# Optimization experiments

Hardware: AMD Instinct MI355X
Metric: run time of the kernel (lower is better)

The kernel has to match this reference:

```python
import jax, jax.numpy as jnp
import numpy as np

B, T, N, F, H, R, E = 32, 8, 150, 16, 32, 4, 16


def _gconv(X, Af, Wf):
    # t-product graph conv (Kilmer t-product = circular conv over relation axis,
    # implemented facewise in the Fourier domain): ifft( fft(adj) @ fft(X) @ fft(W) )
    Xf = jnp.fft.fft(X, axis=-1)                      # [b,n,f,r] complex
    Y = jnp.einsum('nmr,bmfr->bnfr', Af, Xf)          # aggregate over nodes
    Y = jnp.einsum('bnfr,for->bnor', Y, Wf)           # feature transform
    return jnp.fft.ifft(Y, axis=-1).real


def _cell(X, Hs, Af, Wf, Bb):
    # TensorGRUCell. NOTE: faithful to the source, H_tilda reuses conv_hr
    # (conv_hh is defined but never used in the original forward).
    Wxz, Wxr, Wxh, Whz, Whr = Wf
    bz, br, bh = Bb[0], Bb[1], Bb[2]                  # [H,R], broadcasts over [b,n,H,R]
    Z = jax.nn.sigmoid(_gconv(X, Af, Wxz) + _gconv(Hs, Af, Whz) + bz)
    Rg = jax.nn.sigmoid(_gconv(X, Af, Wxr) + _gconv(Hs, Af, Whr) + br)
    Ht = jnp.tanh(_gconv(X, Af, Wxh) + _gconv(Rg * Hs, Af, Whr) + bh)
    return Z * Hs + (1.0 - Z) * Ht


def setup_inputs() -> dict:
    key = jax.random.key(0)
    ks = jax.random.split(key, 16)
    kai = lambda k, shp, fan: (jax.random.normal(k, shp, jnp.float32)
                               * np.float32(np.sqrt(2.0 / fan)))
    d = {}
    d['inputs'] = jax.random.normal(ks[0], (B, T, N, F, R), jnp.float32)
    d['U'] = kai(ks[1], (N, E, R), N)
    # layer 0 (input_dim=F)
    d['Wxz0'] = kai(ks[2], (F, H, R), F)
    d['Wxr0'] = kai(ks[3], (F, H, R), F)
    d['Wxh0'] = kai(ks[4], (F, H, R), F)
    d['Whz0'] = kai(ks[5], (H, H, R), H)
    d['Whr0'] = kai(ks[6], (H, H, R), H)
    d['B0'] = kai(ks[7], (3, H, R), 3)
    # layer 1 (input_dim=H)
    d['Wxz1'] = kai(ks[8], (H, H, R), H)
    d['Wxr1'] = kai(ks[9], (H, H, R), H)
    d['Wxh1'] = kai(ks[10], (H, H, R), H)
    d['Whz1'] = kai(ks[11], (H, H, R), H)
    d['Whr1'] = kai(ks[12], (H, H, R), H)
    d['B1'] = kai(ks[13], (3, H, R), 3)
    return d


def reference(inputs, U, Wxz0, Wxr0, Wxh0, Whz0, Whr0, B0,
              Wxz1, Wxr1, Wxh1, Whz1, Whr1, B1):
    # adaptive adjacency: softmax(relu(tprod(U, U^T)), dim=1)
    Uf = jnp.fft.fft(U, axis=-1)                      # [N,E,R] complex
    A = jnp.fft.ifft(jnp.einsum('ner,mer->nmr', Uf, Uf), axis=-1).real
    adj = jax.nn.softmax(jax.nn.relu(A), axis=1)      # [N,N,R]

    Af = jnp.fft.fft(adj, axis=-1)
    Wf0 = tuple(jnp.fft.fft(w, axis=-1) for w in (Wxz0, Wxr0, Wxh0, Whz0, Whr0))
    Wf1 = tuple(jnp.fft.fft(w, axis=-1) for w in (Wxz1, Wxr1, Wxh1, Whz1, Whr1))

    b, t, n, f, r = inputs.shape
    h = Whz0.shape[0]
    z0 = jnp.zeros((b, n, h, r), inputs.dtype)

    # t = 0: layer1 consumes the *current* layer0 output
    o0 = _cell(inputs[:, 0], z0, Af, Wf0, B0)
    o1 = _cell(o0, z0, Af, Wf1, B1)

    # t > 0: faithful to source, layer1 consumes the *previous timestep's*
    # layer0 output (temp_out[t-1][i-1]) with hidden temp_out[t-1][i].
    def step(carry, Xt):
        p0, p1 = carry
        n0 = _cell(Xt, p0, Af, Wf0, B0)
        n1 = _cell(p0, p1, Af, Wf1, B1)
        return (n0, n1), n1

    Xs = jnp.moveaxis(inputs[:, 1:], 1, 0)            # [T-1,B,N,F,R]
    (c0, c1), ys = jax.lax.scan(step, (o0, o1), Xs)

    out = jnp.concatenate([o1[None], ys], axis=0)     # [T,B,N,H,R]
    out = jnp.moveaxis(out, 0, 1)                     # [B,T,N,H,R]
    h_last = jnp.stack([c0, c1])                      # [L,B,N,H,R]
    return out, h_last
```

## Files before the change

kernel.cpp:

```cpp
#include <hip/hip_runtime.h>
#include <math.h>

#define NN 150
#define BB 32
#define TT 8
#define FF 16
#define HH 32
#define ROWS (NN*BB)
#define NCIN (BB*FF)
#define NCH  (BB*HH)
#define ADJ_LD 160
#define PS_LD 65

#define SZ_ADJF (4*NN*ADJ_LD)
#define SZ_WA0  (4*48*32*4)
#define SZ_WA1  (4*64*32*4)
#define SZ_WB   (32*32*4)
#define SZ_STATE (ROWS*HH*4)
#define SZ_PIN  (4*NN*NCIN)

__device__ __forceinline__ float sigmoidf_(float x){ return 1.f/(1.f+expf(-x)); }

__device__ __forceinline__ float comp_of4(float x0, float x1, float x2, float x3, int c) {
  return c==0 ? (x0+x1+x2+x3) : c==1 ? (x0-x2) : c==2 ? (x3-x1) : (x0-x1+x2-x3);
}


__global__ __launch_bounds__(256) void k_pre(
    const float* __restrict__ U, float* __restrict__ adjF,
    const float* __restrict__ Wxz0, const float* __restrict__ Wxr0, const float* __restrict__ Wxh0,
    const float* __restrict__ Whz0, const float* __restrict__ Whr0,
    const float* __restrict__ Wxz1, const float* __restrict__ Wxr1, const float* __restrict__ Wxh1,
    const float* __restrict__ Whz1, const float* __restrict__ Whr1,
    float* __restrict__ WA0p, float* __restrict__ WA1p,
    float* __restrict__ WB0p, float* __restrict__ WB1p) {
  __shared__ float Ufl[NN*16*4];
  __shared__ float Arow[NN*4];
  __shared__ float red[256];
  __shared__ float mxs[4], isms[4];
  int tid = threadIdx.x;
  if (blockIdx.x < NN) {
    int n = blockIdx.x;
    for (int idx = tid; idx < NN*16; idx += 256) {
      const float* s = U + (size_t)idx*4;
      float x0=s[0], x1=s[1], x2=s[2], x3=s[3];
      Ufl[idx*4+0] = x0+x1+x2+x3;
      Ufl[idx*4+1] = x0-x2;
      Ufl[idx*4+2] = x3-x1;
      Ufl[idx*4+3] = x0-x1+x2-x3;
    }
    __syncthreads();
    if (tid < NN) {
      int m = tid;
      float a0=0, ar=0, ai=0, a2=0;
      #pragma unroll
      for (int e = 0; e < 16; ++e) {
        const float* un = &Ufl[(n*16+e)*4];
        const float* um = &Ufl[(m*16+e)*4];
        a0 += un[0]*um[0];
        ar += un[1]*um[1] - un[2]*um[2];
        ai += un[1]*um[2] + un[2]*um[1];
        a2 += un[3]*um[3];
      }
      float r0 = 0.25f*(a0 + 2.f*ar + a2);
      float r1 = 0.25f*(a0 - 2.f*ai - a2);
      float r2 = 0.25f*(a0 - 2.f*ar + a2);
      float r3 = 0.25f*(a0 + 2.f*ai - a2);
      Arow[m*4+0] = fmaxf(r0, 0.f);
      Arow[m*4+1] = fmaxf(r1, 0.f);
      Arow[m*4+2] = fmaxf(r2, 0.f);
      Arow[m*4+3] = fmaxf(r3, 0.f);
    }
    __syncthreads();
    for (int r = 0; r < 4; ++r) {
      float v = (tid < NN) ? Arow[tid*4+r] : -1e30f;
      red[tid] = v; __syncthreads();
      for (int s = 128; s > 0; s >>= 1) { if (tid < s) red[tid] = fmaxf(red[tid], red[tid+s]); __syncthreads(); }
      if (tid == 0) mxs[r] = red[0];
      __syncthreads();
      float e = (tid < NN) ? expf(Arow[tid*4+r] - mxs[r]) : 0.f;
      red[tid] = e; __syncthreads();
      for (int s = 128; s > 0; s >>= 1) { if (tid < s) red[tid] += red[tid+s]; __syncthreads(); }
      if (tid == 0) isms[r] = 1.f / red[0];
      __syncthreads();
      if (tid < NN) Arow[tid*4+r] = e * isms[r];
      __syncthreads();
    }
    if (tid < NN) {
      int m = tid;
      float e0=Arow[m*4+0], e1=Arow[m*4+1], e2=Arow[m*4+2], e3=Arow[m*4+3];
      size_t base = (size_t)n*ADJ_LD + m;
      size_t cs = (size_t)NN*ADJ_LD;
      adjF[base]      = e0+e1+e2+e3;
      adjF[base+cs]   = e0-e2;
      adjF[base+2*cs] = e3-e1;
      adjF[base+3*cs] = e0-e1+e2-e3;
    } else if (tid < ADJ_LD) {
      size_t base = (size_t)n*ADJ_LD + tid;
      size_t cs = (size_t)NN*ADJ_LD;
      adjF[base] = 0.f; adjF[base+cs] = 0.f; adjF[base+2*cs] = 0.f; adjF[base+3*cs] = 0.f;
    }
    return;
  }
  int idx = (blockIdx.x - NN)*256 + tid;
  const float* src = nullptr;
  float* dst; int didx; int c;
  if (idx < SZ_WA0) {
    c = idx / 6144;
    int rem = idx % 6144;
    int k = rem >> 7, og = (rem >> 2) & 31, q = rem & 3;
    if (q == 0) src = (k < FF) ? Wxz0 + ((size_t)k*HH + og)*4 : Whz0 + ((size_t)(k-FF)*HH + og)*4;
    else if (q == 1) src = (k < FF) ? Wxr0 + ((size_t)k*HH + og)*4 : Whr0 + ((size_t)(k-FF)*HH + og)*4;
    else if (q == 2 && k < FF) src = Wxh0 + ((size_t)k*HH + og)*4;
    dst = WA0p; didx = idx;
  } else if (idx < SZ_WA0 + SZ_WA1) {
    int id = idx - SZ_WA0;
    c = id >> 13;
    int rem = id & 8191;
    int k = rem >> 7, og = (rem >> 2) & 31, q = rem & 3;
    if (q == 0) src = (k < HH) ? Wxz1 + ((size_t)k*HH + og)*4 : Whz1 + ((size_t)(k-HH)*HH + og)*4;
    else if (q == 1) src = (k < HH) ? Wxr1 + ((size_t)k*HH + og)*4 : Whr1 + ((size_t)(k-HH)*HH + og)*4;
    else if (q == 2 && k < HH) src = Wxh1 + ((size_t)k*HH + og)*4;
    dst = WA1p; didx = id;
  } else if (idx < SZ_WA0 + SZ_WA1 + SZ_WB) {
    int id = idx - (SZ_WA0 + SZ_WA1);
    int k = id >> 7, o = (id >> 2) & 31;
    c = id & 3;
    src = Whr0 + ((size_t)k*HH + o)*4;
    dst = WB0p; didx = id;
  } else if (idx < SZ_WA0 + SZ_WA1 + 2*SZ_WB) {
    int id = idx - (SZ_WA0 + SZ_WA1 + SZ_WB);
    int k = id >> 7, o = (id >> 2) & 31;
    c = id & 3;
    src = Whr1 + ((size_t)k*HH + o)*4;
    dst = WB1p; didx = id;
  } else return;
  float v0=0,v1=0,v2=0,v3=0;
  if (src) { v0=src[0]; v1=src[1]; v2=src[2]; v3=src[3]; }
  dst[didx] = comp_of4(v0,v1,v2,v3,c);
}

template<bool RAW>
__device__ __forceinline__ void agg_body(const float* __restrict__ adjF,
                                         const float* __restrict__ X,
                                         const float* __restrict__ inp,
                                         float* __restrict__ P, int ncol,
                                         int tile, int part, int rawt,
                                         float* As, float* Xs, int tid) {
  int kbeg = part ? 96 : 0;
  int kend = part ? NN : 96;
  int n0 = (tile % 5) * 32;
  int col0 = (tile / 5) * 32;
  int ti = tid & 31, tj = tid >> 5;
  int j0 = tj * 4;
  float a0[4]={}, aR[4]={}, aI[4]={}, a2v[4]={};
  float4 pa[4], px[4];

  #define LOAD_A(K0)                                                         \
    _Pragma("unroll")                                                        \
    for (int u = 0; u < 4; ++u) {                                            \
      int e = tid + u*256;                                                   \
      int c = e >> 8, rem = e & 255, i = rem >> 3, kq = rem & 7;             \
      int nn_ = n0 + i;                                                      \
      pa[u] = make_float4(0,0,0,0);                                          \
      if (nn_ < NN) pa[u] = *(const float4*)(adjF + ((size_t)c*NN + nn_)*ADJ_LD + (K0) + kq*4); \
    }
  #define STORE_A()                                                          \
    _Pragma("unroll")                                                        \
    for (int u = 0; u < 4; ++u) {                                            \
      int e = tid + u*256;                                                   \
      int c = e >> 8, rem = e & 255, i = rem >> 3, kq = rem & 7;             \
      As[((kq*4+0)*33 + i)*4 + c] = pa[u].x;                                 \
      As[((kq*4+1)*33 + i)*4 + c] = pa[u].y;                                 \
      As[((kq*4+2)*33 + i)*4 + c] = pa[u].z;                                 \
      As[((kq*4+3)*33 + i)*4 + c] = pa[u].w;                                 \
    }
  #define LOAD_X(K0)                                                         \
    if (RAW) {                                                               \
      int q = tid & 7, kk = tid >> 3;                                        \
      int mm = (K0) + kk;                                                    \
      int col = col0 + q*4;                                                  \
      int b = col >> 4, f = col & 15;                                        \
      px[0]=px[1]=px[2]=px[3]=make_float4(0,0,0,0);                          \
      if (mm < NN) {                                                         \
        const float* s = inp + (((size_t)(b*TT + rawt)*NN + mm)*FF + f)*4;   \
        px[0] = *(const float4*)(s+0);                                       \
        px[1] = *(const float4*)(s+4);                                       \
        px[2] = *(const float4*)(s+8);                                       \
        px[3] = *(const float4*)(s+12);                                      \
      }                                                                      \
    } else {                                                                 \
      _Pragma("unroll")                                                      \
      for (int u = 0; u < 4; ++u) {                                          \
        int e = tid + u*256;                                                 \
        int c = e >> 8, rem = e & 255, kk = rem >> 3, q = rem & 7;           \
        int mm = (K0) + kk;                                                  \
        px[u] = make_float4(0,0,0,0);                                        \
        if (mm < NN) px[u] = *(const float4*)(X + ((size_t)c*NN + mm)*ncol + col0 + q*4); \
      }                                                                      \
    }
  #define STORE_X()                                                          \
    if (RAW) {                                                               \
      int q = tid & 7, kk = tid >> 3;                                        \
      float4 r0 = px[0], r1 = px[1], r2 = px[2], r3 = px[3];                 \
      float4 w;                                                              \
      w = make_float4(r0.x+r0.y+r0.z+r0.w, r1.x+r1.y+r1.z+r1.w, r2.x+r2.y+r2.z+r2.w, r3.x+r3.y+r3.z+r3.w); \
      *(float4*)&Xs[(0*32+kk)*36 + q*4] = w;                                 \
      w = make_float4(r0.x-r0.z, r1.x-r1.z, r2.x-r2.z, r3.x-r3.z);           \
      *(float4*)&Xs[(1*32+kk)*36 + q*4] = w;                                 \
      w = make_float4(r0.w-r0.y, r1.w-r1.y, r2.w-r2.y, r3.w-r3.y);           \
      *(float4*)&Xs[(2*32+kk)*36 + q*4] = w;                                 \
      w = make_float4(r0.x-r0.y+r0.z-r0.w, r1.x-r1.y+r1.z-r1.w, r2.x-r2.y+r2.z-r2.w, r3.x-r3.y+r3.z-r3.w); \
      *(float4*)&Xs[(3*32+kk)*36 + q*4] = w;                                 \
    } else {                                                                 \
      _Pragma("unroll")                                                      \
      for (int u = 0; u < 4; ++u) {                                          \
        int e = tid + u*256;                                                 \
        int c = e >> 8, rem = e & 255, kk = rem >> 3, q = rem & 7;           \
        *(float4*)&Xs[(c*32+kk)*36 + q*4] = px[u];                           \
      }                                                                      \
    }

  LOAD_A(kbeg)
  LOAD_X(kbeg)
  for (int k0 = kbeg; k0 < kend; k0 += 32) {
    STORE_A()
    STORE_X()
    __syncthreads();
    int k0n = k0 + 32;
    if (k0n < kend) {
      LOAD_A(k0n)
      LOAD_X(k0n)
    }
    #pragma unroll 4
    for (int k = 0; k < 32; ++k) {
      float4 a4 = *(float4*)&As[(k*33 + ti)*4];
      float4 x0 = *(float4*)&Xs[(0*32+k)*36 + j0];
      float4 x1 = *(float4*)&Xs[(1*32+k)*36 + j0];
      float4 x2 = *(float4*)&Xs[(2*32+k)*36 + j0];
      float4 x3 = *(float4*)&Xs[(3*32+k)*36 + j0];
      float X0v[4]={x0.x,x0.y,x0.z,x0.w}, X1v[4]={x1.x,x1.y,x1.z,x1.w};
      float X2v[4]={x2.x,x2.y,x2.z,x2.w}, X3v[4]={x3.x,x3.y,x3.z,x3.w};
      #pragma unroll
      for (int j = 0; j < 4; ++j) {
        a0[j]  += a4.x*X0v[j];
        aR[j]  += a4.y*X1v[j] - a4.z*X2v[j];
        aI[j]  += a4.y*X2v[j] + a4.z*X1v[j];
        a2v[j] += a4.w*X3v[j];
      }
    }
    __syncthreads();
  }
  #undef LOAD_A
  #undef STORE_A
  #undef LOAD_X
  #undef STORE_X
  int nn_ = n0 + ti;
  if (nn_ < NN) {
    size_t cs = (size_t)NN*ncol;
    size_t rb = (size_t)nn_*ncol + col0 + j0;
    *(float4*)&P[rb]      = make_float4(a0[0],a0[1],a0[2],a0[3]);
    *(float4*)&P[rb+cs]   = make_float4(aR[0],aR[1],aR[2],aR[3]);
    *(float4*)&P[rb+2*cs] = make_float4(aI[0],aI[1],aI[2],aI[3]);
    *(float4*)&P[rb+3*cs] = make_float4(a2v[0],a2v[1],a2v[2],a2v[3]);
  }
}

#define AGG_AS 4224
#define AGG_XS 4608

__global__ __launch_bounds__(256,4) void k_aggIN(const float* __restrict__ adjF,
                                                 const float* __restrict__ inp,
                                                 float* __restrict__ PIN) {
  __shared__ float As[AGG_AS];
  __shared__ float Xs[AGG_XS];
  int u = blockIdx.x;
  int t = u / 160, rem = u % 160, part = rem / 80, tile = rem % 80;
  float* P = PIN + (size_t)t*2*SZ_PIN + (size_t)part*SZ_PIN;
  agg_body<true>(adjF, nullptr, inp, P, NCIN, tile, part, t, As, Xs, threadIdx.x);
}

struct AggParams {
  const float* X0; const float* X1;
  float* P0; float* P1;
  int base1, njobs, nb;
};
__global__ __launch_bounds__(256,4) void k_agg(AggParams pr, const float* __restrict__ adjF) {
  __shared__ float As[AGG_AS];
  __shared__ float Xs[AGG_XS];
  int bid = blockIdx.x;
  int part = (bid >= pr.nb) ? 1 : 0;
  if (part) bid -= pr.nb;
  const float* X; float* P; int tile;
  if (pr.njobs >= 2 && bid >= pr.base1) { X = pr.X1; P = pr.P1; tile = bid - pr.base1; }
  else { X = pr.X0; P = pr.P0; tile = bid; }
  P += (size_t)part * SZ_STATE;
  agg_body<false>(adjF, X, nullptr, P, NCH, tile, part, -1, As, Xs, threadIdx.x);
}

struct FAJob {
  const float* Px;
  const float* Ph;
  const float* W;
  const float* bias;
  const float* hprev;
  float* Z; float* T1; float* Mf;
  int zh;
};
struct FAParams { FAJob j[2]; };

template<int KTOT, int KX>
__device__ __forceinline__ void fusedA_body(const FAJob& jb, float* Ps, float* Ws) {
  const int row0 = blockIdx.x * 16;
  const int tid = threadIdx.x;
  const int og = tid & 31;
  const int rg = tid >> 5;
  const int r0 = rg*2, r1 = rg*2 + 1;
  const size_t psx = (size_t)4*ROWS*KX;
  const size_t psh = (size_t)4*ROWS*HH;
  constexpr int K4 = KTOT/4;
  for (int e = tid; e < 16*4*K4; e += 256) {
    int k4 = e % K4; int c = (e / K4) & 3; int r = e / (K4*4);
    int k = k4*4;
    int row = row0 + r;
    float4 v;
    if (k < KX) {
      const float* a = &jb.Px[((size_t)c*ROWS + row)*KX + k];
      float4 va = *(const float4*)a;
      float4 vb = *(const float4*)(a + psx);
      v = make_float4(va.x+vb.x, va.y+vb.y, va.z+vb.z, va.w+vb.w);
    } else if (jb.zh) {
      v = make_float4(0,0,0,0);
    } else {
      const float* a = &jb.Ph[((size_t)c*ROWS + row)*HH + (k - KX)];
      float4 va = *(const float4*)a;
      float4 vb = *(const float4*)(a + psh);
      v = make_float4(va.x+vb.x, va.y+vb.y, va.z+vb.z, va.w+vb.w);
    }
    Ps[(r*PS_LD + k+0)*4 + c] = v.x;
    Ps[(r*PS_LD + k+1)*4 + c] = v.y;
    Ps[(r*PS_LD + k+2)*4 + c] = v.z;
    Ps[(r*PS_LD + k+3)*4 + c] = v.w;
  }
  float acc0[2][3]={{0,0,0},{0,0,0}}, accR[2][3]={{0,0,0},{0,0,0}};
  float accI[2][3]={{0,0,0},{0,0,0}}, acc2[2][3]={{0,0,0},{0,0,0}};
  constexpr int NCHK = KTOT/16;
  const float4* Wg = (const float4*)jb.W;
  for (int cc = 0; cc < NCHK; ++cc) {
    __syncthreads();
    #pragma unroll
    for (int u = 0; u < 8; ++u) {
      int f = tid + u*256;
      int c = f >> 9, rem = f & 511;
      float4 v = Wg[((size_t)c*KTOT + cc*16)*32 + rem];
      *(float4*)&Ws[((size_t)c*512 + rem)*4] = v;
    }
    __syncthreads();
    #pragma unroll 4
    for (int kk = 0; kk < 16; ++kk) {
      int k = cc*16 + kk;
      float4 pA = *(float4*)&Ps[(r0*PS_LD + k)*4];
      float4 pB = *(float4*)&Ps[(r1*PS_LD + k)*4];
      float4 w0 = *(float4*)&Ws[((0*16+kk)*32+og)*4];
      float4 w1 = *(float4*)&Ws[((1*16+kk)*32+og)*4];
      float4 w2 = *(float4*)&Ws[((2*16+kk)*32+og)*4];
      float4 w3 = *(float4*)&Ws[((3*16+kk)*32+og)*4];
      float W0v[3]={w0.x,w0.y,w0.z}, W1v[3]={w1.x,w1.y,w1.z};
      float W2v[3]={w2.x,w2.y,w2.z}, W3v[3]={w3.x,w3.y,w3.z};
      #pragma unroll
      for (int q = 0; q < 3; ++q) {
        acc0[0][q] += pA.x*W0v[q];
        acc0[1][q] += pB.x*W0v[q];
        accR[0][q] += pA.y*W1v[q] - pA.z*W2v[q];
        accR[1][q] += pB.y*W1v[q] - pB.z*W2v[q];
        accI[0][q] += pA.y*W2v[q] + pA.z*W1v[q];
        accI[1][q] += pB.y*W2v[q] + pB.z*W1v[q];
        acc2[0][q] += pA.w*W3v[q];
        acc2[1][q] += pB.w*W3v[q];
      }
    }
  }
  const float* bz = jb.bias + (0*HH + og)*4;
  const float* br = jb.bias + (1*HH + og)*4;
  const float* bh = jb.bias + (2*HH + og)*4;
  float bzv[4] = {bz[0],bz[1],bz[2],bz[3]};
  float brv[4] = {br[0],br[1],br[2],br[3]};
  float bhv[4] = {bh[0],bh[1],bh[2],bh[3]};
  #pragma unroll
  for (int rr = 0; rr < 2; ++rr) {
    int row = row0 + rg*2 + rr;
    float ys[3][4];
    #pragma unroll
    for (int q = 0; q < 3; ++q) {
      float Y0 = acc0[rr][q], Yr = accR[rr][q], Yi = accI[rr][q], Y2 = acc2[rr][q];
      ys[q][0] = 0.25f*(Y0 + 2.f*Yr + Y2);
      ys[q][1] = 0.25f*(Y0 - 2.f*Yi - Y2);
      ys[q][2] = 0.25f*(Y0 - 2.f*Yr + Y2);
      ys[q][3] = 0.25f*(Y0 + 2.f*Yi - Y2);
    }
    float4 z = make_float4(sigmoidf_(ys[0][0]+bzv[0]), sigmoidf_(ys[0][1]+bzv[1]),
                           sigmoidf_(ys[0][2]+bzv[2]), sigmoidf_(ys[0][3]+bzv[3]));
    *(float4*)&jb.Z[((size_t)row*HH + og)*4] = z;
    float4 hp = make_float4(0,0,0,0);
    if (!jb.zh) hp = *(const float4*)&jb.hprev[((size_t)row*HH + og)*4];
    float m0 = sigmoidf_(ys[1][0]+brv[0]) * hp.x;
    float m1 = sigmoidf_(ys[1][1]+brv[1]) * hp.y;
    float m2 = sigmoidf_(ys[1][2]+brv[2]) * hp.z;
    float m3 = sigmoidf_(ys[1][3]+brv[3]) * hp.w;
    size_t mb = (size_t)row*HH + og;
    size_t cs = (size_t)ROWS*HH;
    jb.Mf[mb]      = m0+m1+m2+m3;
    jb.Mf[mb+cs]   = m0-m2;
    jb.Mf[mb+2*cs] = m3-m1;
    jb.Mf[mb+3*cs] = m0-m1+m2-m3;
    float4 tv = make_float4(ys[2][0]+bhv[0], ys[2][1]+bhv[1], ys[2][2]+bhv[2], ys[2][3]+bhv[3]);
    *(float4*)&jb.T1[((size_t)row*HH + og)*4] = tv;
  }
}

#define FA_PS (16*PS_LD*4)

__global__ __launch_bounds__(256,3) void k_fusedA_both(FAParams pr) {
  __shared__ float Ps[FA_PS];
  __shared__ float Ws[8192];
  if (blockIdx.y == 0) fusedA_body<48,16>(pr.j[0], Ps, Ws);
  else                 fusedA_body<64,32>(pr.j[1], Ps, Ws);
}
__global__ __launch_bounds__(256,3) void k_fusedA_L0(FAParams pr) {
  __shared__ float Ps[FA_PS];
  __shared__ float Ws[8192];
  fusedA_body<48,16>(pr.j[0], Ps, Ws);
}
__global__ __launch_bounds__(256,3) void k_fusedA_L1(FAParams pr) {
  __shared__ float Ps[FA_PS];
  __shared__ float Ws[8192];
  fusedA_body<64,32>(pr.j[1], Ps, Ws);
}

struct FBJob {
  const float* Pm; const float* W; const float* T1; const float* Z;
  float* h; float* hf; float* outp; float* hlast;
  int t, zh, wout;
};
struct FBParams { FBJob j[2]; };
__global__ __launch_bounds__(256,4) void k_fusedB(FBParams pr) {
  __shared__ float Ps[16*32*4];
  __shared__ float Ws[32*32*4];
  FBJob jb = pr.j[blockIdx.y];
  int row0 = blockIdx.x * 16;
  int tid = threadIdx.x;
  int rg = tid >> 5, o = tid & 31;
  int r0 = rg*2, r1 = r0 + 1;
  float acc0[2]={0,0}, accR[2]={0,0}, accI[2]={0,0}, acc2[2]={0,0};
  if (!jb.zh) {
    #pragma unroll
    for (int u = 0; u < 4; ++u) {
      int f = tid + u*256;
      ((float4*)Ws)[f] = ((const float4*)jb.W)[f];
    }
    const size_t psh = (size_t)4*ROWS*HH;
    #pragma unroll
    for (int u = 0; u < 2; ++u) {
      int e = tid + u*256;
      int r = e >> 5, k = e & 31;
      int row = row0 + r;
      float4 v;
      float* vv = (float*)&v;
      #pragma unroll
      for (int c = 0; c < 4; ++c) {
        size_t ix = ((size_t)c*ROWS + row)*HH + k;
        vv[c] = jb.Pm[ix] + jb.Pm[ix + psh];
      }
      *(float4*)&Ps[(r*32 + k)*4] = v;
    }
    __syncthreads();
    #pragma unroll 8
    for (int k = 0; k < 32; ++k) {
      float4 pA = *(const float4*)&Ps[(r0*32 + k)*4];
      float4 pB = *(const float4*)&Ps[(r1*32 + k)*4];
      float4 w  = *(const float4*)&Ws[(k*32 + o)*4];
      acc0[0] += pA.x*w.x;  acc0[1] += pB.x*w.x;
      accR[0] += pA.y*w.y - pA.z*w.z;  accR[1] += pB.y*w.y - pB.z*w.z;
      accI[0] += pA.y*w.z + pA.z*w.y;  accI[1] += pB.y*w.z + pB.z*w.y;
      acc2[0] += pA.w*w.w;  acc2[1] += pB.w*w.w;
    }
  }
  #pragma unroll
  for (int rr = 0; rr < 2; ++rr) {
    int row = row0 + rg*2 + rr;
    float y0 = 0.25f*(acc0[rr] + 2.f*accR[rr] + acc2[rr]);
    float y1 = 0.25f*(acc0[rr] - 2.f*accI[rr] - acc2[rr]);
    float y2 = 0.25f*(acc0[rr] - 2.f*accR[rr] + acc2[rr]);
    float y3 = 0.25f*(acc0[rr] + 2.f*accI[rr] - acc2[rr]);
    float4 t1 = *(const float4*)&jb.T1[((size_t)row*HH + o)*4];
    float h0v = tanhf(t1.x + y0);
    float h1v = tanhf(t1.y + y1);
    float h2v = tanhf(t1.z + y2);
    float h3v = tanhf(t1.w + y3);
    float4 z = *(const float4*)&jb.Z[((size_t)row*HH + o)*4];
    float4 hp = make_float4(0,0,0,0);
    if (!jb.zh) hp = *(const float4*)&jb.h[((size_t)row*HH + o)*4];
    float n0v = z.x*hp.x + (1.f-z.x)*h0v;
    float n1v = z.y*hp.y + (1.f-z.y)*h1v;
    float n2v = z.z*hp.z + (1.f-z.z)*h2v;
    float n3v = z.w*hp.w + (1.f-z.w)*h3v;
    *(float4*)&jb.h[((size_t)row*HH + o)*4] = make_float4(n0v,n1v,n2v,n3v);
    size_t hb = (size_t)row*HH + o, cs = (size_t)ROWS*HH;
    jb.hf[hb]      = n0v+n1v+n2v+n3v;
    jb.hf[hb+cs]   = n0v-n2v;
    jb.hf[hb+2*cs] = n3v-n1v;
    jb.hf[hb+3*cs] = n0v-n1v+n2v-n3v;
    int n = row >> 5, b = row & 31;
    if (jb.wout) {
      float* dst = jb.outp + (((size_t)b*TT + jb.t)*NN + n)*(HH*4) + o*4;
      *(float4*)dst = make_float4(n0v,n1v,n2v,n3v);
    }
    if (jb.hlast) {
      float* dst = jb.hlast + ((size_t)(b*NN + n))*(HH*4) + o*4;
      *(float4*)dst = make_float4(n0v,n1v,n2v,n3v);
    }
  }
}

extern "C" void kernel_launch(void* const* d_in, const int* in_sizes, int n_in,
                              void* d_out, int out_size, void* d_ws, size_t ws_size,
                              hipStream_t stream) {
  const float* inp  = (const float*)d_in[0];
  const float* U    = (const float*)d_in[1];
  const float* Wxz0 = (const float*)d_in[2];
  const float* Wxr0 = (const float*)d_in[3];
  const float* Wxh0 = (const float*)d_in[4];
  const float* Whz0 = (const float*)d_in[5];
  const float* Whr0 = (const float*)d_in[6];
  const float* B0   = (const float*)d_in[7];
  const float* Wxz1 = (const float*)d_in[8];
  const float* Wxr1 = (const float*)d_in[9];
  const float* Wxh1 = (const float*)d_in[10];
  const float* Whz1 = (const float*)d_in[11];
  const float* Whr1 = (const float*)d_in[12];
  const float* B1   = (const float*)d_in[13];
  float* out = (float*)d_out;

  float* ws = (float*)d_ws;
  float* ADJF = ws;  ws += SZ_ADJF;
  float* WA0  = ws;  ws += SZ_WA0;
  float* WA1  = ws;  ws += SZ_WA1;
  float* WB0  = ws;  ws += SZ_WB;
  float* WB1  = ws;  ws += SZ_WB;
  float* H0   = ws;  ws += SZ_STATE;
  float* H1   = ws;  ws += SZ_STATE;
  float* H0F  = ws;  ws += SZ_STATE;
  float* H1F  = ws;  ws += SZ_STATE;
  float* PIN  = ws;  ws += (size_t)TT*2*SZ_PIN;
  float* PH0  = ws;  ws += 2*SZ_STATE;
  float* PH1  = ws;  ws += 2*SZ_STATE;
  float* PM0  = ws;  ws += 2*SZ_STATE;
  float* PM1  = ws;  ws += 2*SZ_STATE;
  float* M0F  = ws;  ws += SZ_STATE;
  float* M1F  = ws;  ws += SZ_STATE;
  float* Z0   = ws;  ws += SZ_STATE;
  float* Z1   = ws;  ws += SZ_STATE;
  float* T10  = ws;  ws += SZ_STATE;
  float* T11  = ws;  ws += SZ_STATE;

  k_pre<<<NN + (SZ_WA0+SZ_WA1+2*SZ_WB+255)/256, 256, 0, stream>>>(
      U, ADJF, Wxz0,Wxr0,Wxh0,Whz0,Whr0, Wxz1,Wxr1,Wxh1,Whz1,Whr1, WA0,WA1,WB0,WB1);

  k_aggIN<<<TT*2*80, 256, 0, stream>>>(ADJF, inp, PIN);

  float* hlast0 = out + (size_t)BB*TT*NN*HH*4;
  float* hlast1 = hlast0 + (size_t)BB*NN*HH*4;

  {
    FAParams p;
    p.j[0] = FAJob{PIN, nullptr, WA0, B0, nullptr, Z0, T10, M0F, 1};
    p.j[1] = p.j[0];
    k_fusedA_L0<<<dim3(300,1), 256, 0, stream>>>(p);
  }
  {
    FBParams p;
    p.j[0] = FBJob{nullptr, WB0, T10, Z0, H0, H0F, nullptr, nullptr, 0, 1, 0};
    p.j[1] = p.j[0];
    k_fusedB<<<dim3(300,1), 256, 0, stream>>>(p);
  }
  {
    AggParams p; p.X0=H0F; p.P0=PH0; p.X1=nullptr; p.P1=nullptr;
    p.base1=0; p.njobs=1; p.nb=160;
    k_agg<<<320, 256, 0, stream>>>(p, ADJF);
  }
  {
    FAParams p;
    p.j[0] = FAJob{PH0, nullptr, WA1, B1, nullptr, Z1, T11, M1F, 1};
    p.j[1] = p.j[0];
    k_fusedA_L1<<<dim3(300,1), 256, 0, stream>>>(p);
  }
  {
    FBParams p;
    p.j[0] = FBJob{nullptr, WB1, T11, Z1, H1, H1F, out, nullptr, 0, 1, 1};
    p.j[1] = p.j[0];
    k_fusedB<<<dim3(300,1), 256, 0, stream>>>(p);
  }

  for (int t = 1; t < TT; ++t) {
    {
      AggParams p; p.X0=H0F; p.P0=PH0; p.X1=H1F; p.P1=PH1;
      p.base1=160; p.njobs=2; p.nb=320;
      k_agg<<<640, 256, 0, stream>>>(p, ADJF);
    }
    {
      FAParams p;
      p.j[0] = FAJob{PIN + (size_t)t*2*SZ_PIN, PH0, WA0, B0, H0, Z0, T10, M0F, 0};
      p.j[1] = FAJob{PH0, PH1, WA1, B1, H1, Z1, T11, M1F, 0};
      k_fusedA_both<<<dim3(300,2), 256, 0, stream>>>(p);
    }
    {
      AggParams p; p.X0=M0F; p.P0=PM0; p.X1=M1F; p.P1=PM1;
      p.base1=160; p.njobs=2; p.nb=320;
      k_agg<<<640, 256, 0, stream>>>(p, ADJF);
    }
    {
      int last = (t == TT-1);
      FBParams p;
      p.j[0] = FBJob{PM0, WB0, T10, Z0, H0, H0F, nullptr, last ? hlast0 : nullptr, t, 0, 0};
      p.j[1] = FBJob{PM1, WB1, T11, Z1, H1, H1F, out,     last ? hlast1 : nullptr, t, 0, 1};
      k_fusedB<<<dim3(300,2), 256, 0, stream>>>(p);
    }
  }
}
```

Measured before the change: 830.2 us.

## Fuse per-timestep node aggregation with gate GEMMs into two kernels

Each recurrent timestep now runs two fused kernels instead of four. Each one computes the Fourier-domain adjacency aggregation for a 16-node by one-batch tile in shared memory and immediately applies the feature-transform GEMMs and gate nonlinearities for both layers. This removes the global round trips of the partial aggregation buffers and two launches per step. The cost is a full-K aggregation per block without the earlier split-K parallelism, only 320 blocks, lower occupancy (launch bounds of 2) and heavier shared-memory use.

Result: slower. 1.019 ms (+22.8%).

```diff
diff --git a/kernel.cpp b/kernel.cpp
--- a/kernel.cpp
+++ b/kernel.cpp
@@ -281,9 +281,7 @@
 }
 
 struct AggParams {
-  const float* X0; const float* X1;
-  float* P0; float* P1;
-  int base1, njobs, nb;
+  const float* X0; float* P0; int nb;
 };
 __global__ __launch_bounds__(256,4) void k_agg(AggParams pr, const float* __restrict__ adjF) {
   __shared__ float As[AGG_AS];
@@ -291,18 +289,12 @@
   int bid = blockIdx.x;
   int part = (bid >= pr.nb) ? 1 : 0;
   if (part) bid -= pr.nb;
-  const float* X; float* P; int tile;
-  if (pr.njobs >= 2 && bid >= pr.base1) { X = pr.X1; P = pr.P1; tile = bid - pr.base1; }
-  else { X = pr.X0; P = pr.P0; tile = bid; }
-  P += (size_t)part * SZ_STATE;
-  agg_body<false>(adjF, X, nullptr, P, NCH, tile, part, -1, As, Xs, threadIdx.x);
+  float* P = pr.P0 + (size_t)part * SZ_STATE;
+  agg_body<false>(adjF, pr.X0, nullptr, P, NCH, bid, part, -1, As, Xs, threadIdx.x);
 }
 
 struct FAJob {
-  const float* Px;
-  const float* Ph;
-  const float* W;
-  const float* bias;
+  const float* Px; const float* Ph; const float* W; const float* bias;
   const float* hprev;
   float* Z; float* T1; float* Mf;
   int zh;
@@ -420,12 +412,6 @@
 
 #define FA_PS (16*PS_LD*4)
 
-__global__ __launch_bounds__(256,3) void k_fusedA_both(FAParams pr) {
-  __shared__ float Ps[FA_PS];
-  __shared__ float Ws[8192];
-  if (blockIdx.y == 0) fusedA_body<48,16>(pr.j[0], Ps, Ws);
-  else                 fusedA_body<64,32>(pr.j[1], Ps, Ws);
-}
 __global__ __launch_bounds__(256,3) void k_fusedA_L0(FAParams pr) {
   __shared__ float Ps[FA_PS];
   __shared__ float Ws[8192];
@@ -522,6 +508,294 @@
   }
 }
 
+#define SMEM_STEP 11392
+
+__device__ __forceinline__ void step_agg(const float* __restrict__ adjF,
+    const float* __restrict__ X0g, const float* __restrict__ X1g,
+    int n0, int b, int tid, float* smem) {
+  float* As  = smem;
+  float* Xs0 = smem + 2176;
+  float* Xs1 = smem + 6784;
+  int an = tid & 15, hg = (tid >> 4) & 7, job = tid >> 7;
+  int h0 = hg * 4;
+  const float* Xsj = job ? Xs1 : Xs0;
+  float a0[4]={}, aR[4]={}, aI[4]={}, a2[4]={};
+  float4 pa[2], px[8];
+
+  #define SLOAD(K0)                                                          \
+    { _Pragma("unroll") for (int u = 0; u < 2; ++u) {                        \
+        int e = tid + u*256;                                                 \
+        int c = e >> 7, rem = e & 127, i = rem >> 3, kq = rem & 7;           \
+        int nn_ = n0 + i;                                                    \
+        pa[u] = make_float4(0,0,0,0);                                        \
+        if (nn_ < NN) pa[u] = *(const float4*)(adjF + ((size_t)c*NN + nn_)*ADJ_LD + (K0) + kq*4); \
+      }                                                                      \
+      _Pragma("unroll") for (int u = 0; u < 8; ++u) {                        \
+        int e = tid + u*256;                                                 \
+        int jj = e >> 10, rem = e & 1023, c = rem >> 8, rem2 = rem & 255;    \
+        int kk = rem2 >> 3, q = rem2 & 7;                                    \
+        int m = (K0) + kk;                                                   \
+        const float* Xg = jj ? X1g : X0g;                                    \
+        px[u] = make_float4(0,0,0,0);                                       \
+        if (m < NN) px[u] = *(const float4*)(Xg + ((size_t)c*NN + m)*NCH + b*32 + q*4); \
+      } }
+  #define SSTORE()                                                           \
+    { _Pragma("unroll") for (int u = 0; u < 2; ++u) {                        \
+        int e = tid + u*256;                                                 \
+        int c = e >> 7, rem = e & 127, i = rem >> 3, kq = rem & 7;           \
+        As[((kq*4+0)*17 + i)*4 + c] = pa[u].x;                               \
+        As[((kq*4+1)*17 + i)*4 + c] = pa[u].y;                               \
+        As[((kq*4+2)*17 + i)*4 + c] = pa[u].z;                               \
+        As[((kq*4+3)*17 + i)*4 + c] = pa[u].w;                               \
+      }                                                                      \
+      _Pragma("unroll") for (int u = 0; u < 8; ++u) {                        \
+        int e = tid + u*256;                                                 \
+        int jj = e >> 10, rem = e & 1023, c = rem >> 8, rem2 = rem & 255;    \
+        int kk = rem2 >> 3, q = rem2 & 7;                                    \
+        float* Xsd = jj ? Xs1 : Xs0;                                         \
+        *(float4*)&Xsd[(c*32+kk)*36 + q*4] = px[u];                          \
+      } }
+
+  SLOAD(0)
+  for (int k0 = 0; k0 < 160; k0 += 32) {
+    SSTORE()
+    __syncthreads();
+    if (k0 + 32 < 160) SLOAD(k0+32)
+    #pragma unroll 4
+    for (int k = 0; k < 32; ++k) {
+      float4 a4 = *(float4*)&As[(k*17 + an)*4];
+      float4 x0 = *(float4*)&Xsj[(0*32+k)*36 + h0];
+      float4 x1 = *(float4*)&Xsj[(1*32+k)*36 + h0];
+      float4 x2 = *(float4*)&Xsj[(2*32+k)*36 + h0];
+      float4 x3 = *(float4*)&Xsj[(3*32+k)*36 + h0];
+      float X0v[4]={x0.x,x0.y,x0.z,x0.w}, X1v[4]={x1.x,x1.y,x1.z,x1.w};
+      float X2v[4]={x2.x,x2.y,x2.z,x2.w}, X3v[4]={x3.x,x3.y,x3.z,x3.w};
+      #pragma unroll
+      for (int j = 0; j < 4; ++j) {
+        a0[j] += a4.x*X0v[j];
+        aR[j] += a4.y*X1v[j] - a4.z*X2v[j];
+        aI[j] += a4.y*X2v[j] + a4.z*X1v[j];
+        a2[j] += a4.w*X3v[j];
+      }
+    }
+    __syncthreads();
+  }
+  #undef SLOAD
+  #undef SSTORE
+  float* PsH = smem + job*2112;
+  #pragma unroll
+  for (int j = 0; j < 4; ++j)
+    *(float4*)&PsH[(an*33 + h0 + j)*4] = make_float4(a0[j], aR[j], aI[j], a2[j]);
+}
+
+template<int KTOT, int KXA>
+__device__ __forceinline__ void s1_pass(const float* __restrict__ Wraw,
+    const float* __restrict__ bias, const float* __restrict__ hprev,
+    float* __restrict__ Z, float* __restrict__ T1, float* __restrict__ Mf,
+    const float* PsA, int stA, const float* PsB, int stB,
+    float* Ws, int n0, int b, int tid) {
+  const float4* Wg = (const float4*)Wraw;
+  int og = tid & 31, rg = tid >> 5;
+  float acc0[2][3]={{0,0,0},{0,0,0}}, accR[2][3]={{0,0,0},{0,0,0}};
+  float accI[2][3]={{0,0,0},{0,0,0}}, acc2[2][3]={{0,0,0},{0,0,0}};
+  constexpr int NCHK = KTOT/8;
+  for (int cc = 0; cc < NCHK; ++cc) {
+    __syncthreads();
+    #pragma unroll
+    for (int u = 0; u < 4; ++u) {
+      int f = tid + u*256;
+      int c = f >> 8, rem = f & 255, kk = rem >> 5, o = rem & 31;
+      float4 v = Wg[((size_t)c*KTOT + cc*8 + kk)*32 + o];
+      *(float4*)&Ws[((c*8+kk)*32 + o)*4] = v;
+    }
+    __syncthreads();
+    const float* pb; int st, ko;
+    if (cc*8 < KXA) { pb = PsA; st = stA; ko = 0; }
+    else            { pb = PsB; st = stB; ko = KXA; }
+    #pragma unroll 2
+    for (int kk = 0; kk < 8; ++kk) {
+      int k = cc*8 + kk;
+      float4 w0 = *(float4*)&Ws[((0*8+kk)*32+og)*4];
+      float4 w1 = *(float4*)&Ws[((1*8+kk)*32+og)*4];
+      float4 w2 = *(float4*)&Ws[((2*8+kk)*32+og)*4];
+      float4 w3 = *(float4*)&Ws[((3*8+kk)*32+og)*4];
+      float W0v[3]={w0.x,w0.y,w0.z}, W1v[3]={w1.x,w1.y,w1.z};
+      float W2v[3]={w2.x,w2.y,w2.z}, W3v[3]={w3.x,w3.y,w3.z};
+      #pragma unroll
+      for (int rr = 0; rr < 2; ++rr) {
+        int r = rg*2 + rr;
+        float4 p = *(const float4*)&pb[r*st + (k-ko)*4];
+        #pragma unroll
+        for (int q = 0; q < 3; ++q) {
+          acc0[rr][q] += p.x*W0v[q];
+          accR[rr][q] += p.y*W1v[q] - p.z*W2v[q];
+          accI[rr][q] += p.y*W2v[q] + p.z*W1v[q];
+          acc2[rr][q] += p.w*W3v[q];
+        }
+      }
+    }
+  }
+  const float* bz = bias + (0*HH + og)*4;
+  const float* br = bias + (1*HH + og)*4;
+  const float* bh = bias + (2*HH + og)*4;
+  float bzv[4] = {bz[0],bz[1],bz[2],bz[3]};
+  float brv[4] = {br[0],br[1],br[2],br[3]};
+  float bhv[4] = {bh[0],bh[1],bh[2],bh[3]};
+  #pragma unroll
+  for (int rr = 0; rr < 2; ++rr) {
+    int n = n0 + rg*2 + rr;
+    if (n >= NN) continue;
+    int row = n*BB + b;
+    float ys[3][4];
+    #pragma unroll
+    for (int q = 0; q < 3; ++q) {
+      float Y0 = acc0[rr][q], Yr = accR[rr][q], Yi = accI[rr][q], Y2 = acc2[rr][q];
+      ys[q][0] = 0.25f*(Y0 + 2.f*Yr + Y2);
+      ys[q][1] = 0.25f*(Y0 - 2.f*Yi - Y2);
+      ys[q][2] = 0.25f*(Y0 - 2.f*Yr + Y2);
+      ys[q][3] = 0.25f*(Y0 + 2.f*Yi - Y2);
+    }
+    float4 z = make_float4(sigmoidf_(ys[0][0]+bzv[0]), sigmoidf_(ys[0][1]+bzv[1]),
+                           sigmoidf_(ys[0][2]+bzv[2]), sigmoidf_(ys[0][3]+bzv[3]));
+    *(float4*)&Z[((size_t)row*HH + og)*4] = z;
+    float4 hp = *(const float4*)&hprev[((size_t)row*HH + og)*4];
+    float m0 = sigmoidf_(ys[1][0]+brv[0]) * hp.x;
+    float m1 = sigmoidf_(ys[1][1]+brv[1]) * hp.y;
+    float m2 = sigmoidf_(ys[1][2]+brv[2]) * hp.z;
+    float m3 = sigmoidf_(ys[1][3]+brv[3]) * hp.w;
+    size_t mb = (size_t)row*HH + og;
+    size_t cs = (size_t)ROWS*HH;
+    Mf[mb]      = m0+m1+m2+m3;
+    Mf[mb+cs]   = m0-m2;
+    Mf[mb+2*cs] = m3-m1;
+    Mf[mb+3*cs] = m0-m1+m2-m3;
+    float4 tv = make_float4(ys[2][0]+bhv[0], ys[2][1]+bhv[1], ys[2][2]+bhv[2], ys[2][3]+bhv[3]);
+    *(float4*)&T1[((size_t)row*HH + og)*4] = tv;
+  }
+}
+
+struct S1Params {
+  const float* adjF; const float* PINt;
+  const float* H0F; const float* H1F;
+  const float* WA0; const float* WA1;
+  const float* B0; const float* B1;
+  const float* H0; const float* H1;
+  float* Z0; float* T10; float* M0F;
+  float* Z1; float* T11; float* M1F;
+};
+
+__global__ __launch_bounds__(256,2) void k_step1(S1Params p) {
+  __shared__ float smem[SMEM_STEP];
+  int tid = threadIdx.x;
+  int nt = blockIdx.x % 10, b = blockIdx.x / 10;
+  int n0 = nt * 16;
+  step_agg(p.adjF, p.H0F, p.H1F, n0, b, tid, smem);
+  {
+    int c = tid >> 6, rem = tid & 63, nl = rem >> 2, fq = rem & 3;
+    float4 v = make_float4(0,0,0,0);
+    if (n0 + nl < NN) {
+      const float* a = p.PINt + ((size_t)c*NN + n0+nl)*NCIN + b*16 + fq*4;
+      float4 va = *(const float4*)a;
+      float4 vb = *(const float4*)(a + SZ_PIN);
+      v = make_float4(va.x+vb.x, va.y+vb.y, va.z+vb.z, va.w+vb.w);
+    }
+    float* PsIN = smem + 4224;
+    PsIN[(nl*16 + fq*4+0)*4 + c] = v.x;
+    PsIN[(nl*16 + fq*4+1)*4 + c] = v.y;
+    PsIN[(nl*16 + fq*4+2)*4 + c] = v.z;
+    PsIN[(nl*16 + fq*4+3)*4 + c] = v.w;
+  }
+  float* Ws = smem + 5248;
+  s1_pass<48,16>(p.WA0, p.B0, p.H0, p.Z0, p.T10, p.M0F,
+                 smem + 4224, 64, smem, 132, Ws, n0, b, tid);
+  s1_pass<64,32>(p.WA1, p.B1, p.H1, p.Z1, p.T11, p.M1F,
+                 smem, 132, smem + 2112, 132, Ws, n0, b, tid);
+}
+
+__device__ __forceinline__ void s2_pass(const float* __restrict__ WBg,
+    const float* __restrict__ T1g, const float* __restrict__ Zg,
+    float* __restrict__ h, float* __restrict__ hf,
+    float* __restrict__ outp, float* __restrict__ hlast, int t,
+    const float* PsM, float* Ws, int n0, int b, int tid) {
+  int og = tid & 31, rg = tid >> 5;
+  __syncthreads();
+  #pragma unroll
+  for (int u = 0; u < 4; ++u) {
+    int f = tid + u*256;
+    ((float4*)Ws)[f] = ((const float4*)WBg)[f];
+  }
+  __syncthreads();
+  float acc0[2]={0,0}, accR[2]={0,0}, accI[2]={0,0}, acc2[2]={0,0};
+  #pragma unroll 4
+  for (int k = 0; k < 32; ++k) {
+    float4 w = *(const float4*)&Ws[(k*32 + og)*4];
+    #pragma unroll
+    for (int rr = 0; rr < 2; ++rr) {
+      int r = rg*2 + rr;
+      float4 pm = *(const float4*)&PsM[(r*33 + k)*4];
+      acc0[rr] += pm.x*w.x;
+      accR[rr] += pm.y*w.y - pm.z*w.z;
+      accI[rr] += pm.y*w.z + pm.z*w.y;
+      acc2[rr] += pm.w*w.w;
+    }
+  }
+  #pragma unroll
+  for (int rr = 0; rr < 2; ++rr) {
+    int n = n0 + rg*2 + rr;
+    if (n >= NN) continue;
+    int row = n*BB + b;
+    float y0 = 0.25f*(acc0[rr] + 2.f*accR[rr] + acc2[rr]);
+    float y1 = 0.25f*(acc0[rr] - 2.f*accI[rr] - acc2[rr]);
+    float y2 = 0.25f*(acc0[rr] - 2.f*accR[rr] + acc2[rr]);
+    float y3 = 0.25f*(acc0[rr] + 2.f*accI[rr] - acc2[rr]);
+    float4 t1 = *(const float4*)&T1g[((size_t)row*HH + og)*4];
+    float h0v = tanhf(t1.x + y0);
+    float h1v = tanhf(t1.y + y1);
+    float h2v = tanhf(t1.z + y2);
+    float h3v = tanhf(t1.w + y3);
+    float4 z = *(const float4*)&Zg[((size_t)row*HH + og)*4];
+    float4 hp = *(const float4*)&h[((size_t)row*HH + og)*4];
+    float n0v = z.x*hp.x + (1.f-z.x)*h0v;
+    float n1v = z.y*hp.y + (1.f-z.y)*h1v;
+    float n2v = z.z*hp.z + (1.f-z.z)*h2v;
+    float n3v = z.w*hp.w + (1.f-z.w)*h3v;
+    *(float4*)&h[((size_t)row*HH + og)*4] = make_float4(n0v,n1v,n2v,n3v);
+    size_t hb = (size_t)row*HH + og, cs = (size_t)ROWS*HH;
+    hf[hb]      = n0v+n1v+n2v+n3v;
+    hf[hb+cs]   = n0v-n2v;
+    hf[hb+2*cs] = n3v-n1v;
+    hf[hb+3*cs] = n0v-n1v+n2v-n3v;
+    if (outp) {
+      float* dst = outp + (((size_t)b*TT + t)*NN + n)*(HH*4) + og*4;
+      *(float4*)dst = make_float4(n0v,n1v,n2v,n3v);
+    }
+    if (hlast) {
+      float* dst = hlast + ((size_t)(b*NN + n))*(HH*4) + og*4;
+      *(float4*)dst = make_float4(n0v,n1v,n2v,n3v);
+    }
+  }
+}
+
+struct S2Params {
+  const float* adjF; const float* M0F; const float* M1F;
+  const float* WB0; const float* WB1;
+  const float* T10; const float* Z0; const float* T11; const float* Z1;
+  float* H0; float* H1; float* H0F; float* H1F;
+  float* outp; float* hlast0; float* hlast1;
+  int t;
+};
+
+__global__ __launch_bounds__(256,2) void k_step2(S2Params p) {
+  __shared__ float smem[SMEM_STEP];
+  int tid = threadIdx.x;
+  int nt = blockIdx.x % 10, b = blockIdx.x / 10;
+  int n0 = nt * 16;
+  step_agg(p.adjF, p.M0F, p.M1F, n0, b, tid, smem);
+  float* Ws = smem + 4224;
+  s2_pass(p.WB0, p.T10, p.Z0, p.H0, p.H0F, nullptr, p.hlast0, p.t, smem,        Ws, n0, b, tid);
+  s2_pass(p.WB1, p.T11, p.Z1, p.H1, p.H1F, p.outp,  p.hlast1, p.t, smem + 2112, Ws, n0, b, tid);
+}
+
 extern "C" void kernel_launch(void* const* d_in, const int* in_sizes, int n_in,
                               void* d_out, int out_size, void* d_ws, size_t ws_size,
                               hipStream_t stream) {
@@ -553,9 +827,6 @@
   float* H1F  = ws;  ws += SZ_STATE;
   float* PIN  = ws;  ws += (size_t)TT*2*SZ_PIN;
   float* PH0  = ws;  ws += 2*SZ_STATE;
-  float* PH1  = ws;  ws += 2*SZ_STATE;
-  float* PM0  = ws;  ws += 2*SZ_STATE;
-  float* PM1  = ws;  ws += 2*SZ_STATE;
   float* M0F  = ws;  ws += SZ_STATE;
   float* M1F  = ws;  ws += SZ_STATE;
   float* Z0   = ws;  ws += SZ_STATE;
@@ -584,14 +855,13 @@
     k_fusedB<<<dim3(300,1), 256, 0, stream>>>(p);
   }
   {
-    AggParams p; p.X0=H0F; p.P0=PH0; p.X1=nullptr; p.P1=nullptr;
-    p.base1=0; p.njobs=1; p.nb=160;
+    AggParams p; p.X0 = H0F; p.P0 = PH0; p.nb = 160;
     k_agg<<<320, 256, 0, stream>>>(p, ADJF);
   }
   {
     FAParams p;
-    p.j[0] = FAJob{PH0, nullptr, WA1, B1, nullptr, Z1, T11, M1F, 1};
-    p.j[1] = p.j[0];
+    p.j[0] = FAJob{PIN, nullptr, WA0, B0, nullptr, Z0, T10, M0F, 1};
+    p.j[1] = FAJob{PH0, nullptr, WA1, B1, nullptr, Z1, T11, M1F, 1};
     k_fusedA_L1<<<dim3(300,1), 256, 0, stream>>>(p);
   }
   {
@@ -603,27 +873,27 @@
 
   for (int t = 1; t < TT; ++t) {
     {
-      AggParams p; p.X0=H0F; p.P0=PH0; p.X1=H1F; p.P1=PH1;
-      p.base1=160; p.njobs=2; p.nb=320;
-      k_agg<<<640, 256, 0, stream>>>(p, ADJF);
-    }
-    {
-      FAParams p;
-      p.j[0] = FAJob{PIN + (size_t)t*2*SZ_PIN, PH0, WA0, B0, H0, Z0, T10, M0F, 0};
-      p.j[1] = FAJob{PH0, PH1, WA1, B1, H1, Z1, T11, M1F, 0};
-      k_fusedA_both<<<dim3(300,2), 256, 0, stream>>>(p);
-    }
-    {
-      AggParams p; p.X0=M0F; p.P0=PM0; p.X1=M1F; p.P1=PM1;
-      p.base1=160; p.njobs=2; p.nb=320;
-      k_agg<<<640, 256, 0, stream>>>(p, ADJF);
+      S1Params p;
+      p.adjF = ADJF; p.PINt = PIN + (size_t)t*2*SZ_PIN;
+      p.H0F = H0F; p.H1F = H1F;
+      p.WA0 = WA0; p.WA1 = WA1; p.B0 = B0; p.B1 = B1;
+      p.H0 = H0; p.H1 = H1;
+      p.Z0 = Z0; p.T10 = T10; p.M0F = M0F;
+      p.Z1 = Z1; p.T11 = T11; p.M1F = M1F;
+      k_step1<<<320, 256, 0, stream>>>(p);
     }
     {
       int last = (t == TT-1);
-      FBParams p;
-      p.j[0] = FBJob{PM0, WB0, T10, Z0, H0, H0F, nullptr, last ? hlast0 : nullptr, t, 0, 0};
-      p.j[1] = FBJob{PM1, WB1, T11, Z1, H1, H1F, out,     last ? hlast1 : nullptr, t, 0, 1};
-      k_fusedB<<<dim3(300,2), 256, 0, stream>>>(p);
-    }
-  }
-}
+      S2Params p;
+      p.adjF = ADJF; p.M0F = M0F; p.M1F = M1F;
+      p.WB0 = WB0; p.WB1 = WB1;
+      p.T10 = T10; p.Z0 = Z0; p.T11 = T11; p.Z1 = Z1;
+      p.H0 = H0; p.H1 = H1; p.H0F = H0F; p.H1F = H1F;
+      p.outp = out;
+      p.hlast0 = last ? hlast0 : nullptr;
+      p.hlast1 = last ? hlast1 : nullptr;
+      p.t = t;
+      k_step2<<<320, 256, 0, stream>>>(p);
+    }
+  }
+}
```
